# Kernel optimization log

Measured on AMD Instinct MI355X. Metric: run time of the kernel, lower is better.

Reference implementation:

```python
import jax, jax.numpy as jnp
import numpy as np

N = 100000
E = 3200000
IN_DIM = 192
OUT_DIM = 2  # heads=1, out_channels=2
NEG_SLOPE = 0.2


def setup_inputs() -> dict:
    key = jax.random.key(0)
    ks = jax.random.split(key, 7)
    x = jax.random.normal(ks[0], (N, IN_DIM), dtype=jnp.float32)
    edge_index = jax.random.randint(ks[1], (2, E), 0, N, dtype=jnp.int64)
    edge_attr = jax.random.normal(ks[2], (E, 1), dtype=jnp.float32)
    # Glorot-ish scaled params
    W = jax.random.normal(ks[3], (IN_DIM, OUT_DIM), dtype=jnp.float32) * (1.0 / np.sqrt(IN_DIM))
    att_src = jax.random.normal(ks[4], (OUT_DIM,), dtype=jnp.float32)
    att_dst = jax.random.normal(ks[5], (OUT_DIM,), dtype=jnp.float32)
    bias = jax.random.normal(ks[6], (OUT_DIM,), dtype=jnp.float32) * 0.01
    return {"x": x, "edge_index": edge_index, "edge_attr": edge_attr,
            "W": W, "att_src": att_src, "att_dst": att_dst, "bias": bias}


def _gat_conv(x, edge_index, W, att_src, att_dst, bias):
    # Project node features: [N, OUT_DIM]
    x_proj = x @ W
    # Per-node attention logits (heads=1): [N]
    a_src = x_proj @ att_src
    a_dst = x_proj @ att_dst
    # Add self loops (PyG GATConv default add_self_loops=True)
    loop = jnp.arange(N, dtype=edge_index.dtype)
    src = jnp.concatenate([edge_index[0], loop])  # [E+N] message sources j
    dst = jnp.concatenate([edge_index[1], loop])  # [E+N] message targets i
    # Edge attention logits with LeakyReLU
    alpha = a_src[src] + a_dst[dst]
    alpha = jnp.where(alpha >= 0, alpha, NEG_SLOPE * alpha)
    # Segment softmax over incoming edges of each target node
    seg_max = jax.ops.segment_max(alpha, dst, num_segments=N)
    alpha = jnp.exp(alpha - seg_max[dst])
    seg_sum = jax.ops.segment_sum(alpha, dst, num_segments=N)
    alpha = alpha / (seg_sum[dst] + 1e-16)
    # Weighted scatter-aggregate of source features
    msgs = alpha[:, None] * x_proj[src]  # [E+N, OUT_DIM]
    out = jax.ops.segment_sum(msgs, dst, num_segments=N)
    return out + bias


def reference(x, edge_index, edge_attr, W, att_src, att_dst, bias):
    # edge_attr is unpacked in the original forward but never used by conv1
    return _gat_conv(x, edge_index, W, att_src, att_dst, bias)
```

## Files before the change

kernel.cpp:

```cpp
#include <hip/hip_runtime.h>

#define N_NODES 100000
#define N_EDGES 3200000
#define IN_DIM 192
#define NEG_SLOPE 0.2f

#define RSH 8
#define NPR 256
#define NREG2 391
#define EPB 8192
#define P1BLK ((N_EDGES + EPB - 1) / EPB)
#define BST 392
#define CAP2 9216
#define PROJ_WPB 16
#define PROJ_BLOCKS ((N_NODES + PROJ_WPB - 1) / PROJ_WPB)

__global__ __launch_bounds__(1024) void k1_proj_pass1(
    const float* __restrict__ x, const float* __restrict__ W,
    const float* __restrict__ att_src, const float* __restrict__ att_dst,
    float4* __restrict__ node_data, const int* __restrict__ ei,
    unsigned int* __restrict__ ipack, int* __restrict__ boundary)
{
    __shared__ unsigned int vpack[EPB];
    __shared__ int hist[NREG2], lstart[NREG2], rankR[NREG2];
    const int t = threadIdx.x;

    if (blockIdx.x >= P1BLK) {
        const int wave = (blockIdx.x - P1BLK) * PROJ_WPB + (t >> 6);
        const int lane = t & 63;
        if (wave >= N_NODES) return;
        float p0 = 0.f, p1 = 0.f;
        if (lane < 48) {
            const float4 xv = *reinterpret_cast<const float4*>(x + (size_t)wave * IN_DIM + lane * 4);
            const float* Wr = W + lane * 4 * 2;
            p0 = xv.x * Wr[0] + xv.y * Wr[2] + xv.z * Wr[4] + xv.w * Wr[6];
            p1 = xv.x * Wr[1] + xv.y * Wr[3] + xv.z * Wr[5] + xv.w * Wr[7];
        }
        #pragma unroll
        for (int off = 32; off >= 1; off >>= 1) {
            p0 += __shfl_down(p0, off, 64);
            p1 += __shfl_down(p1, off, 64);
        }
        if (lane == 0) {
            const float as = p0 * att_src[0] + p1 * att_src[1];
            const float ad = p0 * att_dst[0] + p1 * att_dst[1];
            node_data[wave] = make_float4(p0, p1, as, ad);
        }
        return;
    }

    for (int i = t; i < NREG2; i += 1024) hist[i] = 0;
    __syncthreads();

    const int e0 = blockIdx.x * EPB;
    const int ecnt = min(EPB, N_EDGES - e0);
    int ss[8], dd[8];
    bool ok[2];
    #pragma unroll
    for (int j = 0; j < 2; ++j) {
        const int e = e0 + (j * 1024 + t) * 4;
        ok[j] = (e < N_EDGES);
        if (ok[j]) {
            const int4 s4 = *reinterpret_cast<const int4*>(ei + e);
            const int4 d4 = *reinterpret_cast<const int4*>(ei + N_EDGES + e);
            ss[j*4+0] = s4.x; ss[j*4+1] = s4.y; ss[j*4+2] = s4.z; ss[j*4+3] = s4.w;
            dd[j*4+0] = d4.x; dd[j*4+1] = d4.y; dd[j*4+2] = d4.z; dd[j*4+3] = d4.w;
            atomicAdd(&hist[d4.x >> RSH], 1);
            atomicAdd(&hist[d4.y >> RSH], 1);
            atomicAdd(&hist[d4.z >> RSH], 1);
            atomicAdd(&hist[d4.w >> RSH], 1);
        }
    }
    __syncthreads();

    if (t < 64) {
        int carry = 0;
        #pragma unroll
        for (int c = 0; c < 7; ++c) {
            const int idx = c * 64 + t;
            const int v = (idx < NREG2) ? hist[idx] : 0;
            int s = v;
            #pragma unroll
            for (int off = 1; off < 64; off <<= 1) {
                const int u = __shfl_up(s, off, 64);
                if (t >= off) s += u;
            }
            if (idx < NREG2) lstart[idx] = carry + s - v;
            carry += __shfl(s, 63, 64);
        }
    }
    __syncthreads();
    if (t < NREG2) {
        rankR[t] = 0;
        boundary[blockIdx.x * BST + t] = lstart[t];
    }
    if (t == NREG2) boundary[blockIdx.x * BST + NREG2] = ecnt;
    __syncthreads();

    #pragma unroll
    for (int j = 0; j < 2; ++j) {
        if (ok[j]) {
            #pragma unroll
            for (int k = 0; k < 4; ++k) {
                const int s = ss[j*4+k], d = dd[j*4+k];
                const int r = d >> RSH;
                const int rk = atomicAdd(&rankR[r], 1);
                vpack[lstart[r] + rk] = ((unsigned int)s << 8) | (unsigned int)(d & 255);
            }
        }
    }
    __syncthreads();

    for (int i4 = t * 4; i4 < ecnt; i4 += 1024 * 4)
        *reinterpret_cast<uint4*>(&ipack[e0 + i4]) =
            *reinterpret_cast<const uint4*>(&vpack[i4]);
}

__global__ __launch_bounds__(1024) void k2_region_agg(
    const unsigned int* __restrict__ ipack, const int* __restrict__ boundary,
    const float4* __restrict__ node_data, const float* __restrict__ bias,
    float* __restrict__ out)
{
    __shared__ unsigned int vals[CAP2];
    __shared__ int slen[P1BLK], sbase[P1BLK];
    __shared__ int spre[P1BLK + 1];
    __shared__ int histN[NPR], startN[NPR], rankN[NPR];
    __shared__ float adst[NPR];
    __shared__ float part0[1024], part1[1024], partw[1024];
    const int r = blockIdx.x, t = threadIdx.x;

    if (t < NPR) {
        const int n = r * NPR + t;
        histN[t] = 0; rankN[t] = 0;
        adst[t] = (n < N_NODES) ? node_data[n].w : 0.f;
    }
    if (t < P1BLK) {
        const int b0 = boundary[t * BST + r];
        const int b1 = boundary[t * BST + r + 1];
        slen[t]  = b1 - b0;
        sbase[t] = t * EPB + b0;
    }
    __syncthreads();

    if (t < 64) {
        int carry = 0;
        #pragma unroll
        for (int c = 0; c < 7; ++c) {
            const int idx = c * 64 + t;
            const int v = (idx < P1BLK) ? slen[idx] : 0;
            int s = v;
            #pragma unroll
            for (int off = 1; off < 64; off <<= 1) {
                const int u = __shfl_up(s, off, 64);
                if (t >= off) s += u;
            }
            if (idx < P1BLK) spre[idx] = carry + s - v;
            carry += __shfl(s, 63, 64);
        }
        if (t == 0) spre[P1BLK] = carry;
    }
    __syncthreads();
    const int total = min(spre[P1BLK], CAP2);

    for (int s2 = t; s2 < P1BLK; s2 += 1024) {
        int b0 = spre[s2];
        int len = slen[s2];
        if (b0 < CAP2) {
            if (b0 + len > CAP2) len = CAP2 - b0;
            const int gb = sbase[s2];
            for (int k = 0; k < len; ++k) vals[b0 + k] = (unsigned int)(gb + k);
        }
    }
    __syncthreads();

    unsigned int ent[9];
    int nl[9];
    #pragma unroll
    for (int j = 0; j < 9; ++j) {
        const int i = t + j * 1024;
        if (i < total) {
            const unsigned int e = ipack[vals[i]];
            ent[j] = e >> 8;
            nl[j]  = (int)(e & 255u);
            atomicAdd(&histN[nl[j]], 1);
        } else nl[j] = -1;
    }
    __syncthreads();

    if (t < 64) {
        int carry = 0;
        #pragma unroll
        for (int c2 = 0; c2 < 4; ++c2) {
            const int idx = c2 * 64 + t;
            const int v = histN[idx];
            int s = v;
            #pragma unroll
            for (int off = 1; off < 64; off <<= 1) {
                const int u = __shfl_up(s, off, 64);
                if (t >= off) s += u;
            }
            startN[idx] = carry + s - v;
            carry += __shfl(s, 63, 64);
        }
    }
    __syncthreads();

    #pragma unroll
    for (int j = 0; j < 9; ++j) {
        if (nl[j] >= 0) {
            const int rk = atomicAdd(&rankN[nl[j]], 1);
            vals[startN[nl[j]] + rk] = ent[j];
        }
    }
    __syncthreads();

    {
        const int node = t & 255, sl = t >> 8;
        const float ad = adst[node];
        const int rs = startN[node], re = rs + histN[node];
        float s0 = 0.f, s1 = 0.f, sw = 0.f;
        for (int i = rs + sl; i < re; i += 4) {
            const int src = (int)vals[i];
            const float4 nd = node_data[src];
            float a = nd.z + ad;
            a = (a >= 0.f) ? a : NEG_SLOPE * a;
            const float w = __expf(a);
            s0 += w * nd.x; s1 += w * nd.y; sw += w;
        }
        part0[t] = s0; part1[t] = s1; partw[t] = sw;
    }
    __syncthreads();

    if (t < NPR) {
        const int n = r * NPR + t;
        if (n < N_NODES) {
            const float A0 = part0[t] + part0[t + 256] + part0[t + 512] + part0[t + 768];
            const float A1 = part1[t] + part1[t + 256] + part1[t + 512] + part1[t + 768];
            const float AW = partw[t] + partw[t + 256] + partw[t + 512] + partw[t + 768];
            const float4 nd = node_data[n];
            float a = nd.z + nd.w;
            a = (a >= 0.f) ? a : NEG_SLOPE * a;
            const float w = __expf(a);
            const float den = AW + w + 1e-16f;
            const float o0 = (A0 + w * nd.x) / den + bias[0];
            const float o1 = (A1 + w * nd.y) / den + bias[1];
            *reinterpret_cast<float2*>(out + (size_t)n * 2) = make_float2(o0, o1);
        }
    }
}

__global__ __launch_bounds__(256) void proj_kernel(
    const float* __restrict__ x, const float* __restrict__ W,
    const float* __restrict__ att_src, const float* __restrict__ att_dst,
    float4* __restrict__ node_data, float4* __restrict__ accum)
{
    const int wave = (blockIdx.x * blockDim.x + threadIdx.x) >> 6;
    const int lane = threadIdx.x & 63;
    if (wave >= N_NODES) return;
    float p0 = 0.f, p1 = 0.f;
    if (lane < 48) {
        const float4 xv = *reinterpret_cast<const float4*>(x + (size_t)wave * IN_DIM + lane * 4);
        const float* Wr = W + lane * 4 * 2;
        p0 = xv.x * Wr[0] + xv.y * Wr[2] + xv.z * Wr[4] + xv.w * Wr[6];
        p1 = xv.x * Wr[1] + xv.y * Wr[3] + xv.z * Wr[5] + xv.w * Wr[7];
    }
    #pragma unroll
    for (int off = 32; off >= 1; off >>= 1) {
        p0 += __shfl_down(p0, off, 64);
        p1 += __shfl_down(p1, off, 64);
    }
    if (lane == 0) {
        const float as = p0 * att_src[0] + p1 * att_src[1];
        const float ad = p0 * att_dst[0] + p1 * att_dst[1];
        node_data[wave] = make_float4(p0, p1, as, ad);
        if (accum) accum[wave] = make_float4(0.f, 0.f, 0.f, 0.f);
    }
}

__global__ __launch_bounds__(256) void edge_kernel_atomic(
    const int* __restrict__ ei, const float4* __restrict__ node_data,
    float* __restrict__ accum)
{
    const int t = blockIdx.x * blockDim.x + threadIdx.x;
    const int base = t * 4;
    if (base >= N_EDGES) return;
    const int4 s4 = *reinterpret_cast<const int4*>(ei + base);
    const int4 d4 = *reinterpret_cast<const int4*>(ei + N_EDGES + base);
    const int ss[4] = {s4.x, s4.y, s4.z, s4.w};
    const int dd[4] = {d4.x, d4.y, d4.z, d4.w};
    #pragma unroll
    for (int k = 0; k < 4; ++k) {
        const int s = ss[k], d = dd[k];
        const float4 nds = node_data[s];
        const float ad = reinterpret_cast<const float*>(node_data)[d * 4 + 3];
        float a = nds.z + ad;
        a = (a >= 0.f) ? a : NEG_SLOPE * a;
        const float w = __expf(a);
        atomicAdd(&accum[d * 4 + 0], w * nds.x);
        atomicAdd(&accum[d * 4 + 1], w * nds.y);
        atomicAdd(&accum[d * 4 + 2], w);
    }
}

__global__ __launch_bounds__(256) void finalize_kernel(
    const float4* __restrict__ node_data, const float4* __restrict__ accum,
    const float* __restrict__ bias, float* __restrict__ out)
{
    const int n = blockIdx.x * blockDim.x + threadIdx.x;
    if (n >= N_NODES) return;
    const float4 nd = node_data[n];
    const float4 ac = accum[n];
    float a = nd.z + nd.w;
    a = (a >= 0.f) ? a : NEG_SLOPE * a;
    const float w = __expf(a);
    const float den = ac.z + w + 1e-16f;
    const float o0 = (ac.x + w * nd.x) / den + bias[0];
    const float o1 = (ac.y + w * nd.y) / den + bias[1];
    *reinterpret_cast<float2*>(out + (size_t)n * 2) = make_float2(o0, o1);
}

extern "C" void kernel_launch(void* const* d_in, const int* in_sizes, int n_in,
                              void* d_out, int out_size, void* d_ws, size_t ws_size,
                              hipStream_t stream) {
    const float* x       = (const float*)d_in[0];
    const int*   ei      = (const int*)d_in[1];
    const float* W       = (const float*)d_in[3];
    const float* att_src = (const float*)d_in[4];
    const float* att_dst = (const float*)d_in[5];
    const float* bias    = (const float*)d_in[6];
    float* out = (float*)d_out;

    char* p = (char*)d_ws;
    float4* node_data = (float4*)p;            p += (size_t)N_NODES * 16;
    unsigned int* ipack = (unsigned int*)p;    p += (size_t)P1BLK * EPB * 4;
    int* boundary = (int*)p;                   p += (size_t)P1BLK * BST * 4;
    const size_t need = (size_t)(p - (char*)d_ws);

    if (ws_size >= need) {
        k1_proj_pass1<<<P1BLK + PROJ_BLOCKS, 1024, 0, stream>>>(
            x, W, att_src, att_dst, node_data, ei, ipack, boundary);
        k2_region_agg<<<NREG2, 1024, 0, stream>>>(ipack, boundary, node_data, bias, out);
    } else {
        float4* nd2 = (float4*)d_ws;
        float4* accum = nd2 + N_NODES;
        proj_kernel<<<(N_NODES + 3) / 4, 256, 0, stream>>>(x, W, att_src, att_dst, nd2, accum);
        edge_kernel_atomic<<<(N_EDGES / 4 + 255) / 256, 256, 0, stream>>>(ei, nd2, (float*)accum);
        finalize_kernel<<<(N_NODES + 255) / 256, 256, 0, stream>>>(nd2, accum, bias, out);
    }
}
```

Before: 58.40 us.

## Shrink binning blocks to 2048 edges and pack per-region offset/count into one word

The first kernel now sorts 2048 edges per 512-thread block instead of 8192 per 1024-thread block, giving four times as many, smaller blocks for better occupancy and load balance. Each block's per-region start offset and count are packed into one 32-bit word, so the aggregation kernel reads one value per segment instead of two adjacent boundaries. The trade-off is that the aggregation kernel must now gather and prefix-scan about 1563 segment descriptors per region instead of 391, adding work and scattered reads in that stage.

```diff
diff --git a/kernel.cpp b/kernel.cpp
--- a/kernel.cpp
+++ b/kernel.cpp
@@ -8,18 +8,19 @@
 #define RSH 8
 #define NPR 256
 #define NREG2 391
-#define EPB 8192
+
+#define EPB 2048
 #define P1BLK ((N_EDGES + EPB - 1) / EPB)
-#define BST 392
+#define BROW 400
 #define CAP2 9216
-#define PROJ_WPB 16
+#define PROJ_WPB 8
 #define PROJ_BLOCKS ((N_NODES + PROJ_WPB - 1) / PROJ_WPB)
 
-__global__ __launch_bounds__(1024) void k1_proj_pass1(
+__global__ __launch_bounds__(512) void k1_proj_pass1(
     const float* __restrict__ x, const float* __restrict__ W,
     const float* __restrict__ att_src, const float* __restrict__ att_dst,
     float4* __restrict__ node_data, const int* __restrict__ ei,
-    unsigned int* __restrict__ ipack, int* __restrict__ boundary)
+    unsigned int* __restrict__ ipack, unsigned int* __restrict__ bpack)
 {
     __shared__ unsigned int vpack[EPB];
     __shared__ int hist[NREG2], lstart[NREG2], rankR[NREG2];
@@ -49,27 +50,23 @@
         return;
     }
 
-    for (int i = t; i < NREG2; i += 1024) hist[i] = 0;
+    for (int i = t; i < NREG2; i += 512) hist[i] = 0;
     __syncthreads();
 
     const int e0 = blockIdx.x * EPB;
     const int ecnt = min(EPB, N_EDGES - e0);
-    int ss[8], dd[8];
-    bool ok[2];
-    #pragma unroll
-    for (int j = 0; j < 2; ++j) {
-        const int e = e0 + (j * 1024 + t) * 4;
-        ok[j] = (e < N_EDGES);
-        if (ok[j]) {
-            const int4 s4 = *reinterpret_cast<const int4*>(ei + e);
-            const int4 d4 = *reinterpret_cast<const int4*>(ei + N_EDGES + e);
-            ss[j*4+0] = s4.x; ss[j*4+1] = s4.y; ss[j*4+2] = s4.z; ss[j*4+3] = s4.w;
-            dd[j*4+0] = d4.x; dd[j*4+1] = d4.y; dd[j*4+2] = d4.z; dd[j*4+3] = d4.w;
-            atomicAdd(&hist[d4.x >> RSH], 1);
-            atomicAdd(&hist[d4.y >> RSH], 1);
-            atomicAdd(&hist[d4.z >> RSH], 1);
-            atomicAdd(&hist[d4.w >> RSH], 1);
-        }
+    const int e = e0 + t * 4;
+    const bool ok = (e < N_EDGES);
+    int ss[4], dd[4];
+    if (ok) {
+        const int4 s4 = *reinterpret_cast<const int4*>(ei + e);
+        const int4 d4 = *reinterpret_cast<const int4*>(ei + N_EDGES + e);
+        ss[0] = s4.x; ss[1] = s4.y; ss[2] = s4.z; ss[3] = s4.w;
+        dd[0] = d4.x; dd[1] = d4.y; dd[2] = d4.z; dd[3] = d4.w;
+        atomicAdd(&hist[d4.x >> RSH], 1);
+        atomicAdd(&hist[d4.y >> RSH], 1);
+        atomicAdd(&hist[d4.z >> RSH], 1);
+        atomicAdd(&hist[d4.w >> RSH], 1);
     }
     __syncthreads();
 
@@ -92,32 +89,30 @@
     __syncthreads();
     if (t < NREG2) {
         rankR[t] = 0;
-        boundary[blockIdx.x * BST + t] = lstart[t];
-    }
-    if (t == NREG2) boundary[blockIdx.x * BST + NREG2] = ecnt;
-    __syncthreads();
-
-    #pragma unroll
-    for (int j = 0; j < 2; ++j) {
-        if (ok[j]) {
-            #pragma unroll
-            for (int k = 0; k < 4; ++k) {
-                const int s = ss[j*4+k], d = dd[j*4+k];
-                const int r = d >> RSH;
-                const int rk = atomicAdd(&rankR[r], 1);
-                vpack[lstart[r] + rk] = ((unsigned int)s << 8) | (unsigned int)(d & 255);
-            }
-        }
-    }
-    __syncthreads();
-
-    for (int i4 = t * 4; i4 < ecnt; i4 += 1024 * 4)
+        bpack[(size_t)blockIdx.x * BROW + t] =
+            (unsigned int)lstart[t] | ((unsigned int)hist[t] << 16);
+    }
+    __syncthreads();
+
+    if (ok) {
+        #pragma unroll
+        for (int k = 0; k < 4; ++k) {
+            const int s = ss[k], d = dd[k];
+            const int r = d >> RSH;
+            const int rk = atomicAdd(&rankR[r], 1);
+            vpack[lstart[r] + rk] = ((unsigned int)s << 8) | (unsigned int)(d & 255);
+        }
+    }
+    __syncthreads();
+
+    const int i4 = t * 4;
+    if (i4 < ecnt)
         *reinterpret_cast<uint4*>(&ipack[e0 + i4]) =
             *reinterpret_cast<const uint4*>(&vpack[i4]);
 }
 
 __global__ __launch_bounds__(1024) void k2_region_agg(
-    const unsigned int* __restrict__ ipack, const int* __restrict__ boundary,
+    const unsigned int* __restrict__ ipack, const unsigned int* __restrict__ bpack,
     const float4* __restrict__ node_data, const float* __restrict__ bias,
     float* __restrict__ out)
 {
@@ -134,18 +129,17 @@
         histN[t] = 0; rankN[t] = 0;
         adst[t] = (n < N_NODES) ? node_data[n].w : 0.f;
     }
-    if (t < P1BLK) {
-        const int b0 = boundary[t * BST + r];
-        const int b1 = boundary[t * BST + r + 1];
-        slen[t]  = b1 - b0;
-        sbase[t] = t * EPB + b0;
+    for (int s2 = t; s2 < P1BLK; s2 += 1024) {
+        const unsigned int v = bpack[(size_t)s2 * BROW + r];
+        slen[s2]  = (int)(v >> 16);
+        sbase[s2] = s2 * EPB + (int)(v & 0xFFFFu);
     }
     __syncthreads();
 
     if (t < 64) {
         int carry = 0;
         #pragma unroll
-        for (int c = 0; c < 7; ++c) {
+        for (int c = 0; c < (P1BLK + 63) / 64; ++c) {
             const int idx = c * 64 + t;
             const int v = (idx < P1BLK) ? slen[idx] : 0;
             int s = v;
@@ -333,13 +327,13 @@
     char* p = (char*)d_ws;
     float4* node_data = (float4*)p;            p += (size_t)N_NODES * 16;
     unsigned int* ipack = (unsigned int*)p;    p += (size_t)P1BLK * EPB * 4;
-    int* boundary = (int*)p;                   p += (size_t)P1BLK * BST * 4;
+    unsigned int* bpack = (unsigned int*)p;    p += (size_t)P1BLK * BROW * 4;
     const size_t need = (size_t)(p - (char*)d_ws);
 
     if (ws_size >= need) {
-        k1_proj_pass1<<<P1BLK + PROJ_BLOCKS, 1024, 0, stream>>>(
-            x, W, att_src, att_dst, node_data, ei, ipack, boundary);
-        k2_region_agg<<<NREG2, 1024, 0, stream>>>(ipack, boundary, node_data, bias, out);
+        k1_proj_pass1<<<P1BLK + PROJ_BLOCKS, 512, 0, stream>>>(
+            x, W, att_src, att_dst, node_data, ei, ipack, bpack);
+        k2_region_agg<<<NREG2, 1024, 0, stream>>>(ipack, bpack, node_data, bias, out);
     } else {
         float4* nd2 = (float4*)d_ws;
         float4* accum = nd2 + N_NODES;
```

Measured after the change: 65.79 us. 12.7% more time.
